# Optimization experiments

Hardware: AMD Instinct MI355X
Metric: run time of the kernel (lower is better)

Reference implementation:

```python
import jax, jax.numpy as jnp
import numpy as np

VOCAB = 21128; EMBED = 768; D_MODEL = 256; H = 100; NTAGS = 21; B = 32; T = 256


def setup_inputs() -> dict:
    key = jax.random.key(0)
    ks = jax.random.split(key, 18)
    n = lambda k, s, sc=0.05: jax.random.normal(k, s, dtype=jnp.float32) * sc
    return {
        "words": jax.random.randint(ks[0], (B, T), 0, VOCAB),
        "target": jax.random.randint(ks[1], (B, T), 0, NTAGS),
        "embed_table": n(ks[2], (VOCAB, EMBED), 1.0),
        "in_fc_w": n(ks[3], (D_MODEL, EMBED)),
        "in_fc_b": n(ks[4], (D_MODEL,)),
        "Wih0": n(ks[5], (2, 4 * H, D_MODEL)),
        "Whh0": n(ks[6], (2, 4 * H, H)),
        "bih0": n(ks[7], (2, 4 * H)),
        "bhh0": n(ks[8], (2, 4 * H)),
        "Wih1": n(ks[9], (2, 4 * H, 2 * H)),
        "Whh1": n(ks[10], (2, 4 * H, H)),
        "bih1": n(ks[11], (2, 4 * H)),
        "bhh1": n(ks[12], (2, 4 * H)),
        "out_w": n(ks[13], (NTAGS, 2 * H)),
        "out_b": n(ks[14], (NTAGS,)),
        "trans": n(ks[15], (NTAGS, NTAGS)),
        "start_s": n(ks[16], (NTAGS,)),
        "end_s": n(ks[17], (NTAGS,)),
    }


def _lstm_dir(x, Wih, Whh, bih, bhh, reverse):
    # x: (T, B, D); torch LSTM gate order i, f, g, o
    Bsz, Hd = x.shape[1], Whh.shape[1]
    pre = jnp.einsum('tbd,gd->tbg', x, Wih) + bih  # precompute input projection

    def step(carry, p):
        h, c = carry
        g = p + h @ Whh.T + bhh
        i, f, gg, o = jnp.split(g, 4, axis=-1)
        c = jax.nn.sigmoid(f) * c + jax.nn.sigmoid(i) * jnp.tanh(gg)
        h = jax.nn.sigmoid(o) * jnp.tanh(c)
        return (h, c), h

    init = (jnp.zeros((Bsz, Hd), x.dtype), jnp.zeros((Bsz, Hd), x.dtype))
    _, hs = jax.lax.scan(step, init, pre, reverse=reverse)
    return hs


def _bilstm(x, layers):
    h = x
    for (Wih, Whh, bih, bhh) in layers:  # fixed small loop over num_layers
        f = _lstm_dir(h, Wih[0], Whh[0], bih[0], bhh[0], False)
        b = _lstm_dir(h, Wih[1], Whh[1], bih[1], bhh[1], True)
        h = jnp.concatenate([f, b], axis=-1)
    return h


def _crf_loss(logits, tags, mask, trans, start_s, end_s):
    # fastNLP ConditionalRandomField loss: normalizer - gold_score, per batch elem
    lt = jnp.swapaxes(logits, 0, 1)          # (T, B, N)
    tt = tags.T                               # (T, B)
    mt = mask.T.astype(logits.dtype)          # (T, B)
    alpha0 = lt[0] + start_s

    def step(alpha, inp):
        emit, m = inp
        tmp = alpha[:, :, None] + trans[None] + emit[:, None, :]  # (B, N, N)
        new = jax.nn.logsumexp(tmp, axis=1)
        return jnp.where(m[:, None] > 0, new, alpha), None

    alpha, _ = jax.lax.scan(step, alpha0, (lt[1:], mt[1:]))
    normalizer = jax.nn.logsumexp(alpha + end_s, axis=1)  # (B,)

    emit_sc = jnp.take_along_axis(lt, tt[..., None], axis=2)[..., 0] * mt
    trans_sc = trans[tt[:-1], tt[1:]] * mt[1:]
    seq_lens = mask.sum(axis=1)
    last_idx = jnp.maximum(seq_lens - 1, 0)
    last_tags = tags[jnp.arange(tags.shape[0]), last_idx]
    gold = emit_sc.sum(0) + trans_sc.sum(0) + start_s[tt[0]] + end_s[last_tags]
    return normalizer - gold


def reference(words, target, embed_table, in_fc_w, in_fc_b, Wih0, Whh0, bih0, bhh0,
              Wih1, Whh1, bih1, bhh1, out_w, out_b, trans, start_s, end_s):
    mask = words != 0
    x = embed_table[words]                       # (B, T, E)
    x = x @ in_fc_w.T + in_fc_b                  # (B, T, D)
    x = jnp.swapaxes(x, 0, 1)                    # (T, B, D)
    h = _bilstm(x, [(Wih0, Whh0, bih0, bhh0), (Wih1, Whh1, bih1, bhh1)])
    h = jnp.swapaxes(h, 0, 1)                    # (B, T, 2H); dropout is identity at eval
    logits = jax.nn.log_softmax(h @ out_w.T + out_b, axis=-1)
    return _crf_loss(logits, target, mask, trans, start_s, end_s)  # (B,)
```

## Files before the change

kernel.cpp:

```cpp
#include <hip/hip_runtime.h>
#include <hip/hip_bf16.h>

#define VOCAB 21128
#define EMBED 768
#define DMODEL 256
#define HID 100
#define NTAGS 21
#define BB 32
#define TT 256
#define NTOK (BB*TT)

typedef float f32x4 __attribute__((ext_vector_type(4)));
typedef unsigned int u32x4 __attribute__((ext_vector_type(4)));
typedef short s16x8 __attribute__((ext_vector_type(8)));

__device__ __forceinline__ float sigm(float x) { return 1.0f / (1.0f + __expf(-x)); }
__device__ __forceinline__ float tanh_(float x) { return 2.0f / (1.0f + __expf(-2.0f * x)) - 1.0f; }

__device__ __forceinline__ unsigned int bfr(float x) {
    unsigned int u = __float_as_uint(x);
    return (u + 0x7fffu + ((u >> 16) & 1u)) >> 16;
}
__device__ __forceinline__ unsigned int bfpack(float lo, float hi) {
    return (bfr(hi) << 16) | bfr(lo);
}
__device__ __forceinline__ s16x8 asfrag(u32x4 v) {
    union { u32x4 u; s16x8 s; } x; x.u = v; return x.s;
}

#define BARV(SB) do { \
    asm volatile("s_waitcnt lgkmcnt(0)" ::: "memory"); \
    __builtin_amdgcn_s_barrier(); \
    if (SB) __builtin_amdgcn_sched_barrier(0); \
} while (0)
#define BAR() BARV(1)

__global__ __launch_bounds__(256) void gemm_mfma(
    const float* __restrict__ A, int lda,
    const float* __restrict__ B, int ldb,
    const float* __restrict__ bias1, const float* __restrict__ bias2,
    float* __restrict__ C, int ldc,
    int N, int K,
    const int* __restrict__ gatherWords, int permGates)
{
    __shared__ unsigned int As_[2][4096];
    __shared__ unsigned int Bs_[2][2048];

    const int tid = threadIdx.x;
    const int row0 = blockIdx.x * 128;
    const int col0 = blockIdx.y * 64;
    const int lane = tid & 63;
    const int wave = tid >> 6;
    const int wr = wave >> 1, wc = wave & 1;
    const int nsteps = (K + 63) >> 6;

    const float* arow[8]; int aoff[8]; int kqA[8];
    #pragma unroll
    for (int j = 0; j < 8; ++j) {
        int v = tid + 256 * j;
        int row = v >> 4, kq = v & 15;
        int grow = row0 + row;
        const float* ap;
        if (gatherWords) {
            int widx = gatherWords[(grow & 31) * TT + (grow >> 5)];
            ap = A + (size_t)widx * lda;
        } else {
            ap = A + (size_t)grow * lda;
        }
        arow[j] = ap + 4 * kq;
        aoff[j] = (row >> 4) * 512 + (kq >> 3) * 256 + ((kq >> 1) & 3) * 64
                + (row & 15) * 4 + (kq & 1) * 2;
        kqA[j] = kq;
    }
    const float* brow[4]; int boff[4]; int bok[4]; int kqB[4];
    #pragma unroll
    for (int j = 0; j < 4; ++j) {
        int v = tid + 256 * j;
        int r = v >> 4, kq = v & 15;
        int gcol = col0 + r;
        bok[j] = (gcol < N);
        int src = bok[j] ? gcol : 0;
        if (permGates && bok[j]) {
            int d2 = (gcol >= 400) ? 1 : 0;
            int rr = gcol - d2 * 400;
            src = d2 * 400 + (rr & 3) * 100 + (rr >> 2);
        }
        brow[j] = B + (size_t)src * ldb + 4 * kq;
        boff[j] = (r >> 4) * 512 + (kq >> 3) * 256 + ((kq >> 1) & 3) * 64
                + (r & 15) * 4 + (kq & 1) * 2;
        kqB[j] = kq;
    }

    {
        #pragma unroll
        for (int j = 0; j < 8; ++j) {
            f32x4 v = {0.f,0.f,0.f,0.f};
            if (4 * kqA[j] < K) v = *(const f32x4*)(arow[j]);
            As_[0][aoff[j]]     = bfpack(v.x, v.y);
            As_[0][aoff[j] + 1] = bfpack(v.z, v.w);
        }
        #pragma unroll
        for (int j = 0; j < 4; ++j) {
            f32x4 v = {0.f,0.f,0.f,0.f};
            if (bok[j] && 4 * kqB[j] < K) v = *(const f32x4*)(brow[j]);
            Bs_[0][boff[j]]     = bfpack(v.x, v.y);
            Bs_[0][boff[j] + 1] = bfpack(v.z, v.w);
        }
    }
    BAR();

    f32x4 acc[4][2] = {};

    for (int s = 0; s < nsteps; ++s) {
        const int cur = s & 1, nxt = cur ^ 1;

        f32x4 la[8], lb[4];
        if (s + 1 < nsteps) {
            const int kb = (s + 1) * 64;
            #pragma unroll
            for (int j = 0; j < 8; ++j) {
                la[j] = (f32x4){0.f,0.f,0.f,0.f};
                if (kb + 4 * kqA[j] < K) la[j] = *(const f32x4*)(arow[j] + kb);
            }
            #pragma unroll
            for (int j = 0; j < 4; ++j) {
                lb[j] = (f32x4){0.f,0.f,0.f,0.f};
                if (bok[j] && kb + 4 * kqB[j] < K) lb[j] = *(const f32x4*)(brow[j] + kb);
            }
        }

        u32x4 af[2][4], bf2[2][2];
        #pragma unroll
        for (int f = 0; f < 2; ++f) {
            #pragma unroll
            for (int mt = 0; mt < 4; ++mt)
                af[f][mt] = *(const u32x4*)&As_[cur][(4 * wr + mt) * 512 + f * 256 + lane * 4];
            #pragma unroll
            for (int nt = 0; nt < 2; ++nt)
                bf2[f][nt] = *(const u32x4*)&Bs_[cur][(2 * wc + nt) * 512 + f * 256 + lane * 4];
        }
        #pragma unroll
        for (int f = 0; f < 2; ++f)
            #pragma unroll
            for (int mt = 0; mt < 4; ++mt)
                #pragma unroll
                for (int nt = 0; nt < 2; ++nt)
                    acc[mt][nt] = __builtin_amdgcn_mfma_f32_16x16x32_bf16(
                        asfrag(af[f][mt]), asfrag(bf2[f][nt]), acc[mt][nt], 0, 0, 0);

        if (s + 1 < nsteps) {
            #pragma unroll
            for (int j = 0; j < 8; ++j) {
                As_[nxt][aoff[j]]     = bfpack(la[j].x, la[j].y);
                As_[nxt][aoff[j] + 1] = bfpack(la[j].z, la[j].w);
            }
            #pragma unroll
            for (int j = 0; j < 4; ++j) {
                Bs_[nxt][boff[j]]     = bfpack(lb[j].x, lb[j].y);
                Bs_[nxt][boff[j] + 1] = bfpack(lb[j].z, lb[j].w);
            }
        }
        BAR();
    }

    const int r4 = (lane >> 4) * 4;
    const int cl = lane & 15;
    #pragma unroll
    for (int nt = 0; nt < 2; ++nt) {
        int gcol = col0 + (2 * wc + nt) * 16 + cl;
        if (gcol < N) {
            int src = gcol;
            if (permGates) {
                int d2 = (gcol >= 400) ? 1 : 0;
                int rr = gcol - d2 * 400;
                src = d2 * 400 + (rr & 3) * 100 + (rr >> 2);
            }
            float bv = bias1[src];
            if (bias2) bv += bias2[src];
            #pragma unroll
            for (int mt = 0; mt < 4; ++mt) {
                int grow = row0 + (4 * wr + mt) * 16 + r4;
                #pragma unroll
                for (int r = 0; r < 4; ++r)
                    C[(size_t)(grow + r) * ldc + gcol] = acc[mt][nt][r] + bv;
            }
        }
    }
}

#define STASH_FRAG(DD, F, A0,A1,A2,A3) { \
    int tile = 4*wave + DD; if (tile > 24) tile = 24; \
    int row16 = 16*tile + m16; \
    const float* srcp = Whh + (size_t)(dir*400 + (row16 & 3)*100 + (row16 >> 2)) * HID; \
    const int k0 = 32*F + 8*g4; \
    f32x4 fa = {0.f,0.f,0.f,0.f}, fb = {0.f,0.f,0.f,0.f}; \
    if (k0 < HID) fa = *(const f32x4*)(srcp + k0); \
    if (k0 + 4 < HID) fb = *(const f32x4*)(srcp + k0 + 4); \
    unsigned p0 = bfpack(fa.x, fa.y), p1 = bfpack(fa.z, fa.w); \
    unsigned p2 = bfpack(fb.x, fb.y), p3 = bfpack(fb.z, fb.w); \
    asm volatile("v_accvgpr_write_b32 a" #A0 ", %0\n\t" \
                 "v_accvgpr_write_b32 a" #A1 ", %1\n\t" \
                 "v_accvgpr_write_b32 a" #A2 ", %2\n\t" \
                 "v_accvgpr_write_b32 a" #A3 ", %3" \
                 :: "v"(p0), "v"(p1), "v"(p2), "v"(p3) \
                 : "a" #A0, "a" #A1, "a" #A2, "a" #A3); }

#define MF(ACC, BF, A0, A3) \
    asm volatile("v_mfma_f32_16x16x32_bf16 %0, a[" #A0 ":" #A3 "], %1, %0" \
                 : "+v"(ACC) : "v"(BF));

#define LOADCHUNK(K2) { \
    const int s0_ = 16 * (K2); \
    _Pragma("unroll") \
    for (int j = 0; j < 4; ++j) { \
        if (okj[j]) { \
            int tg = dir ? (TT - 1 - (s0_ + sicj[j])) : (s0_ + sicj[j]); \
            rr[j] = *(const f32x4*)(pre + (size_t)(tg * BB + b) * 800 + dir * 400 + 4 * gqj[j]); \
        } \
    } }

#define WRITECHUNK(BUF) { \
    _Pragma("unroll") \
    for (int j = 0; j < 4; ++j) { \
        if (okj[j]) *(f32x4*)&preS[(BUF) * 6400 + sicj[j] * 400 + 4 * gqj[j]] = rr[j]; \
    } }

#define LSTM_STEP(SIC) { \
    const int t_ = dir ? (TT - 1 - (s0 + (SIC))) : (s0 + (SIC)); \
    const int i_ = t_ * BB + b; \
    const u32x4* hb_ = (const u32x4*)&h16[(SIC) & 1][0]; \
    u32x4 bf0 = hb_[g4], bf1 = hb_[4+g4], bf2 = hb_[8+g4], bf3 = hb_[12+g4]; \
    f32x4 p4 = *(const f32x4*)&preS[curbase + (SIC) * 400 + my_po]; \
    f32x4 acc0 = {0.f,0.f,0.f,0.f}, acc1 = {0.f,0.f,0.f,0.f}; \
    f32x4 acc2 = {0.f,0.f,0.f,0.f}, acc3 = {0.f,0.f,0.f,0.f}; \
    asm volatile("s_nop 1"); \
    MF(acc0, bf0, 0, 3)   MF(acc1, bf0, 16, 19) MF(acc2, bf0, 32, 35) MF(acc3, bf0, 48, 51) \
    MF(acc0, bf1, 4, 7)   MF(acc1, bf1, 20, 23) MF(acc2, bf1, 36, 39) MF(acc3, bf1, 52, 55) \
    MF(acc0, bf2, 8, 11)  MF(acc1, bf2, 24, 27) MF(acc2, bf2, 40, 43) MF(acc3, bf2, 56, 59) \
    MF(acc0, bf3, 12, 15) MF(acc1, bf3, 28, 31) MF(acc2, bf3, 44, 47) MF(acc3, bf3, 60, 63) \
    asm volatile("s_nop 7\n\ts_nop 7"); \
    f32x4 sel = (d == 0) ? acc0 : (d == 1) ? acc1 : (d == 2) ? acc2 : acc3; \
    float igt = sigm(sel.x + p4.x); \
    float fgt = sigm(sel.y + p4.y); \
    float ggt = tanh_(sel.z + p4.z); \
    float ogt = sigm(sel.w + p4.w); \
    c = fgt * c + igt * ggt; \
    float h = ogt * tanh_(c); \
    if (writer) { \
        h16[((SIC) + 1) & 1][my_u] = (unsigned short)bfr(h); \
        hout[(size_t)i_ * 200 + dir * HID + my_u] = h; \
    } \
    BARV(VAR == 0); }

template<int VAR>
__global__ __launch_bounds__(448, 1) void lstm_mfma(
    const float* __restrict__ pre,
    const float* __restrict__ Whh,
    float* __restrict__ hout)
{
    const int dir = blockIdx.x >> 5;
    const int b = blockIdx.x & 31;
    const int tid = threadIdx.x;
    const int wave = tid >> 6;
    const int lane = tid & 63;
    const int m16 = lane & 15;
    const int g4 = lane >> 4;
    const int d = lane & 3;

    __shared__ alignas(16) unsigned short h16[2][128];
    __shared__ alignas(16) float preS[2 * 6400];

    STASH_FRAG(0,0, 0,1,2,3)    STASH_FRAG(0,1, 4,5,6,7)
    STASH_FRAG(0,2, 8,9,10,11)  STASH_FRAG(0,3, 12,13,14,15)
    STASH_FRAG(1,0, 16,17,18,19) STASH_FRAG(1,1, 20,21,22,23)
    STASH_FRAG(1,2, 24,25,26,27) STASH_FRAG(1,3, 28,29,30,31)
    STASH_FRAG(2,0, 32,33,34,35) STASH_FRAG(2,1, 36,37,38,39)
    STASH_FRAG(2,2, 40,41,42,43) STASH_FRAG(2,3, 44,45,46,47)
    STASH_FRAG(3,0, 48,49,50,51) STASH_FRAG(3,1, 52,53,54,55)
    STASH_FRAG(3,2, 56,57,58,59) STASH_FRAG(3,3, 60,61,62,63)

    if (tid < 128) { h16[0][tid] = 0; h16[1][tid] = 0; }

    int my_tile = 4 * wave + d; if (my_tile > 24) my_tile = 24;
    const int my_u = my_tile * 4 + g4;
    const int my_po = 16 * my_tile + 4 * g4;
    const bool writer = ((lane & 12) == 0) && (wave < 6 || d == 0);

    int sicj[4], gqj[4]; bool okj[4];
    #pragma unroll
    for (int j = 0; j < 4; ++j) {
        int idx = tid + 448 * j;
        okj[j] = (idx < 1600);
        int ic = okj[j] ? idx : 0;
        sicj[j] = ic / 100;
        gqj[j] = ic - 100 * sicj[j];
    }

    float c = 0.f;
    f32x4 rr[4];

    LOADCHUNK(0)
    WRITECHUNK(0)
    LOADCHUNK(1)
    BAR();

    for (int k = 0; k < 16; ++k) {
        const int s0 = 16 * k;
        const int curbase = (k & 1) * 6400;
        LSTM_STEP(0)  LSTM_STEP(1)  LSTM_STEP(2)  LSTM_STEP(3)
        LSTM_STEP(4)  LSTM_STEP(5)  LSTM_STEP(6)  LSTM_STEP(7)
        LSTM_STEP(8)  LSTM_STEP(9)  LSTM_STEP(10) LSTM_STEP(11)
        LSTM_STEP(12) LSTM_STEP(13) LSTM_STEP(14) LSTM_STEP(15)
        if (k < 15) { WRITECHUNK((k & 1) ^ 1) }
        if (k < 14) { LOADCHUNK(k + 2) }
        BAR();
    }
}

__global__ __launch_bounds__(256) void logits_lsm(
    const float* __restrict__ h1,
    const float* __restrict__ out_w,
    const float* __restrict__ out_b,
    float* __restrict__ logits)
{
    const int lane = threadIdx.x & 63;
    const int wid = (blockIdx.x * 256 + threadIdx.x) >> 6;
    const int half = lane >> 5;
    const int n = lane & 31;
    const int i = wid * 2 + half;
    if (i >= NTOK) return;

    float acc = -1e30f;
    if (n < NTAGS) {
        acc = out_b[n];
        const float4* hr = (const float4*)(h1 + (size_t)i * 200);
        const float4* wr = (const float4*)(out_w + (size_t)n * 200);
        #pragma unroll
        for (int e = 0; e < 50; ++e) {
            float4 h4 = hr[e], w4 = wr[e];
            acc += h4.x * w4.x + h4.y * w4.y + h4.z * w4.z + h4.w * w4.w;
        }
    }
    float m = acc;
    for (int off = 16; off > 0; off >>= 1) m = fmaxf(m, __shfl_xor(m, off, 32));
    float ex = (n < NTAGS) ? __expf(acc - m) : 0.f;
    float s = ex;
    for (int off = 16; off > 0; off >>= 1) s += __shfl_xor(s, off, 32);
    if (n < NTAGS) logits[(size_t)i * NTAGS + n] = acc - m - __logf(s);
}

__global__ __launch_bounds__(64) void crf_kernel(
    const float* __restrict__ logits,
    const int* __restrict__ words,
    const int* __restrict__ target,
    const float* __restrict__ trans,
    const float* __restrict__ start_s,
    const float* __restrict__ end_s,
    float* __restrict__ out)
{
    const int b = blockIdx.x;
    const int j = threadIdx.x;
    const int j21 = (j < NTAGS) ? j : (NTAGS - 1);

    float tcol[NTAGS];
    #pragma unroll
    for (int i = 0; i < NTAGS; ++i) tcol[i] = (j < NTAGS) ? trans[i * NTAGS + j] : 0.f;

    const int w0 = words[b * TT +   0 + j];
    const int w1 = words[b * TT +  64 + j];
    const int w2 = words[b * TT + 128 + j];
    const int w3 = words[b * TT + 192 + j];

    float alpha = (j < NTAGS) ? (logits[(size_t)(0 * BB + b) * NTAGS + j] + start_s[j]) : -1e30f;
    float e_cur = logits[(size_t)(1 * BB + b) * NTAGS + j21];

#define CRF_CHUNK(WREG, T0) \
    for (int u = ((T0) == 0 ? 1 : 0); u < 64; ++u) { \
        const int t = (T0) + u; \
        float e_nxt = 0.f; \
        if (t + 1 < TT) e_nxt = logits[(size_t)((t + 1) * BB + b) * NTAGS + j21]; \
        if (__shfl(WREG, u, 64) != 0) { \
            float v[NTAGS]; \
            _Pragma("unroll") \
            for (int i2 = 0; i2 < NTAGS; ++i2) \
                v[i2] = __shfl(alpha, i2, 64) + tcol[i2]; \
            float m0[11]; \
            _Pragma("unroll") \
            for (int p = 0; p < 10; ++p) m0[p] = fmaxf(v[2*p], v[2*p+1]); \
            m0[10] = v[20]; \
            float m1[6]; \
            _Pragma("unroll") \
            for (int p = 0; p < 5; ++p) m1[p] = fmaxf(m0[2*p], m0[2*p+1]); \
            m1[5] = m0[10]; \
            float m2a = fmaxf(m1[0], m1[1]), m2b = fmaxf(m1[2], m1[3]), m2c = fmaxf(m1[4], m1[5]); \
            float mx = fmaxf(fmaxf(m2a, m2b), m2c); \
            float e[NTAGS]; \
            _Pragma("unroll") \
            for (int i2 = 0; i2 < NTAGS; ++i2) e[i2] = __expf(v[i2] - mx); \
            float s0[11]; \
            _Pragma("unroll") \
            for (int p = 0; p < 10; ++p) s0[p] = e[2*p] + e[2*p+1]; \
            s0[10] = e[20]; \
            float s1[6]; \
            _Pragma("unroll") \
            for (int p = 0; p < 5; ++p) s1[p] = s0[2*p] + s0[2*p+1]; \
            s1[5] = s0[10]; \
            float ss = ((s1[0] + s1[1]) + (s1[2] + s1[3])) + (s1[4] + s1[5]); \
            float na = mx + __logf(ss) + e_cur; \
            alpha = (j < NTAGS) ? na : -1e30f; \
        } \
        e_cur = e_nxt; \
    }

    CRF_CHUNK(w0, 0)
    CRF_CHUNK(w1, 64)
    CRF_CHUNK(w2, 128)
    CRF_CHUNK(w3, 192)
#undef CRF_CHUNK

    float val = (j < NTAGS) ? (alpha + end_s[j]) : -1e30f;
    float mx = val;
    for (int off = 32; off > 0; off >>= 1) mx = fmaxf(mx, __shfl_xor(mx, off, 64));
    float s = (j < NTAGS) ? __expf(val - mx) : 0.f;
    for (int off = 32; off > 0; off >>= 1) s += __shfl_xor(s, off, 64);
    float norm = mx + __logf(s);

    float gold = 0.f, slen = 0.f;
    for (int t = j; t < TT; t += 64) {
        int tg = target[b * TT + t];
        bool m = (words[b * TT + t] != 0);
        if (m) {
            gold += logits[(size_t)(t * BB + b) * NTAGS + tg];
            slen += 1.f;
            if (t >= 1) gold += trans[target[b * TT + t - 1] * NTAGS + tg];
        }
    }
    for (int off = 32; off > 0; off >>= 1) {
        gold += __shfl_xor(gold, off, 64);
        slen += __shfl_xor(slen, off, 64);
    }
    if (j == 0) {
        int len = (int)slen;
        int last = (len > 0) ? (len - 1) : 0;
        int last_tag = target[b * TT + last];
        gold += start_s[target[b * TT + 0]] + end_s[last_tag];
        out[b] = norm - gold;
    }
}

extern "C" void kernel_launch(void* const* d_in, const int* in_sizes, int n_in,
                              void* d_out, int out_size, void* d_ws, size_t ws_size,
                              hipStream_t stream) {
    const int*   words   = (const int*)  d_in[0];
    const int*   target  = (const int*)  d_in[1];
    const float* embed   = (const float*)d_in[2];
    const float* in_fc_w = (const float*)d_in[3];
    const float* in_fc_b = (const float*)d_in[4];
    const float* Wih0    = (const float*)d_in[5];
    const float* Whh0    = (const float*)d_in[6];
    const float* bih0    = (const float*)d_in[7];
    const float* bhh0    = (const float*)d_in[8];
    const float* Wih1    = (const float*)d_in[9];
    const float* Whh1    = (const float*)d_in[10];
    const float* bih1    = (const float*)d_in[11];
    const float* bhh1    = (const float*)d_in[12];
    const float* out_w   = (const float*)d_in[13];
    const float* out_b   = (const float*)d_in[14];
    const float* trans   = (const float*)d_in[15];
    const float* start_s = (const float*)d_in[16];
    const float* end_s   = (const float*)d_in[17];
    float* out = (float*)d_out;

    float* ws = (float*)d_ws;
    float* x      = ws;
    float* pre    = ws + 2097152;
    float* h0     = ws + 8650752;
    float* h1     = ws;
    float* logits = ws + 1638400;

    gemm_mfma<<<dim3(64, 4), 256, 0, stream>>>(
        embed, EMBED, in_fc_w, EMBED, in_fc_b, nullptr,
        x, DMODEL, DMODEL, EMBED, words, 0);

    gemm_mfma<<<dim3(64, 13), 256, 0, stream>>>(
        x, DMODEL, Wih0, DMODEL, bih0, bhh0,
        pre, 800, 800, DMODEL, nullptr, 1);

    lstm_mfma<0><<<64, 448, 0, stream>>>(pre, Whh0, h0);

    gemm_mfma<<<dim3(64, 13), 256, 0, stream>>>(
        h0, 200, Wih1, 200, bih1, bhh1,
        pre, 800, 800, 200, nullptr, 1);

    lstm_mfma<1><<<64, 448, 0, stream>>>(pre, Whh1, h1);

    logits_lsm<<<NTOK / 8, 256, 0, stream>>>(h1, out_w, out_b, logits);

    crf_kernel<<<BB, 64, 0, stream>>>(logits, words, target, trans, start_s, end_s, out);
}
```

Before: 582.6 us.

## Shrink LSTM recurrence block to 4 waves with 7 MFMA tiles per wave

The recurrent LSTM kernel moves from 7 waves (448 threads, 4 gate tiles each) to 4 waves (256 threads) that each own 6–7 of the 25 16-row Whh tiles, kept in AGPRs. Fewer waves makes the per-timestep block barrier cheaper, at the cost of a longer serial MFMA chain per wave (28 instead of 16) and more AGPR and register pressure. The preactivation chunk loader now does 7 loads per thread instead of 4, and the template variant that disabled the sched barrier is removed.

```diff
diff --git a/kernel.cpp b/kernel.cpp
--- a/kernel.cpp
+++ b/kernel.cpp
@@ -28,12 +28,11 @@
     union { u32x4 u; s16x8 s; } x; x.u = v; return x.s;
 }
 
-#define BARV(SB) do { \
+#define BAR() do { \
     asm volatile("s_waitcnt lgkmcnt(0)" ::: "memory"); \
     __builtin_amdgcn_s_barrier(); \
-    if (SB) __builtin_amdgcn_sched_barrier(0); \
+    __builtin_amdgcn_sched_barrier(0); \
 } while (0)
-#define BAR() BARV(1)
 
 __global__ __launch_bounds__(256) void gemm_mfma(
     const float* __restrict__ A, int lda,
@@ -188,11 +187,11 @@
     }
 }
 
-#define STASH_FRAG(DD, F, A0,A1,A2,A3) { \
-    int tile = 4*wave + DD; if (tile > 24) tile = 24; \
+#define STASH_FRAG(SS, F, A0,A1,A2,A3) { \
+    int tile = base + (SS); if (tile > 24) tile = 24; \
     int row16 = 16*tile + m16; \
     const float* srcp = Whh + (size_t)(dir*400 + (row16 & 3)*100 + (row16 >> 2)) * HID; \
-    const int k0 = 32*F + 8*g4; \
+    const int k0 = 32*(F) + 8*g4; \
     f32x4 fa = {0.f,0.f,0.f,0.f}, fb = {0.f,0.f,0.f,0.f}; \
     if (k0 < HID) fa = *(const f32x4*)(srcp + k0); \
     if (k0 + 4 < HID) fb = *(const f32x4*)(srcp + k0 + 4); \
@@ -212,7 +211,7 @@
 #define LOADCHUNK(K2) { \
     const int s0_ = 16 * (K2); \
     _Pragma("unroll") \
-    for (int j = 0; j < 4; ++j) { \
+    for (int j = 0; j < 7; ++j) { \
         if (okj[j]) { \
             int tg = dir ? (TT - 1 - (s0_ + sicj[j])) : (s0_ + sicj[j]); \
             rr[j] = *(const f32x4*)(pre + (size_t)(tg * BB + b) * 800 + dir * 400 + 4 * gqj[j]); \
@@ -221,7 +220,7 @@
 
 #define WRITECHUNK(BUF) { \
     _Pragma("unroll") \
-    for (int j = 0; j < 4; ++j) { \
+    for (int j = 0; j < 7; ++j) { \
         if (okj[j]) *(f32x4*)&preS[(BUF) * 6400 + sicj[j] * 400 + 4 * gqj[j]] = rr[j]; \
     } }
 
@@ -233,13 +232,28 @@
     f32x4 p4 = *(const f32x4*)&preS[curbase + (SIC) * 400 + my_po]; \
     f32x4 acc0 = {0.f,0.f,0.f,0.f}, acc1 = {0.f,0.f,0.f,0.f}; \
     f32x4 acc2 = {0.f,0.f,0.f,0.f}, acc3 = {0.f,0.f,0.f,0.f}; \
+    f32x4 acc4 = {0.f,0.f,0.f,0.f}, acc5 = {0.f,0.f,0.f,0.f}; \
+    f32x4 acc6 = {0.f,0.f,0.f,0.f}; \
     asm volatile("s_nop 1"); \
-    MF(acc0, bf0, 0, 3)   MF(acc1, bf0, 16, 19) MF(acc2, bf0, 32, 35) MF(acc3, bf0, 48, 51) \
-    MF(acc0, bf1, 4, 7)   MF(acc1, bf1, 20, 23) MF(acc2, bf1, 36, 39) MF(acc3, bf1, 52, 55) \
-    MF(acc0, bf2, 8, 11)  MF(acc1, bf2, 24, 27) MF(acc2, bf2, 40, 43) MF(acc3, bf2, 56, 59) \
-    MF(acc0, bf3, 12, 15) MF(acc1, bf3, 28, 31) MF(acc2, bf3, 44, 47) MF(acc3, bf3, 60, 63) \
+    MF(acc0, bf0, 0, 3)    MF(acc1, bf0, 16, 19)  MF(acc2, bf0, 32, 35) \
+    MF(acc3, bf0, 48, 51)  MF(acc4, bf0, 64, 67)  MF(acc5, bf0, 80, 83) \
+    MF(acc6, bf0, 96, 99) \
+    MF(acc0, bf1, 4, 7)    MF(acc1, bf1, 20, 23)  MF(acc2, bf1, 36, 39) \
+    MF(acc3, bf1, 52, 55)  MF(acc4, bf1, 68, 71)  MF(acc5, bf1, 84, 87) \
+    MF(acc6, bf1, 100, 103) \
+    MF(acc0, bf2, 8, 11)   MF(acc1, bf2, 24, 27)  MF(acc2, bf2, 40, 43) \
+    MF(acc3, bf2, 56, 59)  MF(acc4, bf2, 72, 75)  MF(acc5, bf2, 88, 91) \
+    MF(acc6, bf2, 104, 107) \
+    MF(acc0, bf3, 12, 15)  MF(acc1, bf3, 28, 31)  MF(acc2, bf3, 44, 47) \
+    MF(acc3, bf3, 60, 63)  MF(acc4, bf3, 76, 79)  MF(acc5, bf3, 92, 95) \
+    MF(acc6, bf3, 108, 111) \
     asm volatile("s_nop 7\n\ts_nop 7"); \
-    f32x4 sel = (d == 0) ? acc0 : (d == 1) ? acc1 : (d == 2) ? acc2 : acc3; \
+    f32x4 t01 = (slot_sel & 1) ? acc1 : acc0; \
+    f32x4 t23 = (slot_sel & 1) ? acc3 : acc2; \
+    f32x4 t45 = (slot_sel & 1) ? acc5 : acc4; \
+    f32x4 u0 = (slot_sel & 2) ? t23 : t01; \
+    f32x4 u1 = (slot_sel & 2) ? acc6 : t45; \
+    f32x4 sel = (slot_sel & 4) ? u1 : u0; \
     float igt = sigm(sel.x + p4.x); \
     float fgt = sigm(sel.y + p4.y); \
     float ggt = tanh_(sel.z + p4.z); \
@@ -250,10 +264,9 @@
         h16[((SIC) + 1) & 1][my_u] = (unsigned short)bfr(h); \
         hout[(size_t)i_ * 200 + dir * HID + my_u] = h; \
     } \
-    BARV(VAR == 0); }
-
-template<int VAR>
-__global__ __launch_bounds__(448, 1) void lstm_mfma(
+    BAR(); }
+
+__global__ __launch_bounds__(256, 1) void lstm_mfma(
     const float* __restrict__ pre,
     const float* __restrict__ Whh,
     float* __restrict__ hout)
@@ -265,31 +278,41 @@
     const int lane = tid & 63;
     const int m16 = lane & 15;
     const int g4 = lane >> 4;
-    const int d = lane & 3;
+    const int slot_sel = lane & 7;
+
+    const int base = (wave == 0) ? 0 : (wave == 1) ? 7 : (wave == 2) ? 13 : 19;
 
     __shared__ alignas(16) unsigned short h16[2][128];
     __shared__ alignas(16) float preS[2 * 6400];
 
-    STASH_FRAG(0,0, 0,1,2,3)    STASH_FRAG(0,1, 4,5,6,7)
-    STASH_FRAG(0,2, 8,9,10,11)  STASH_FRAG(0,3, 12,13,14,15)
-    STASH_FRAG(1,0, 16,17,18,19) STASH_FRAG(1,1, 20,21,22,23)
-    STASH_FRAG(1,2, 24,25,26,27) STASH_FRAG(1,3, 28,29,30,31)
-    STASH_FRAG(2,0, 32,33,34,35) STASH_FRAG(2,1, 36,37,38,39)
-    STASH_FRAG(2,2, 40,41,42,43) STASH_FRAG(2,3, 44,45,46,47)
-    STASH_FRAG(3,0, 48,49,50,51) STASH_FRAG(3,1, 52,53,54,55)
-    STASH_FRAG(3,2, 56,57,58,59) STASH_FRAG(3,3, 60,61,62,63)
+    STASH_FRAG(0,0, 0,1,2,3)      STASH_FRAG(0,1, 4,5,6,7)
+    STASH_FRAG(0,2, 8,9,10,11)    STASH_FRAG(0,3, 12,13,14,15)
+    STASH_FRAG(1,0, 16,17,18,19)  STASH_FRAG(1,1, 20,21,22,23)
+    STASH_FRAG(1,2, 24,25,26,27)  STASH_FRAG(1,3, 28,29,30,31)
+    STASH_FRAG(2,0, 32,33,34,35)  STASH_FRAG(2,1, 36,37,38,39)
+    STASH_FRAG(2,2, 40,41,42,43)  STASH_FRAG(2,3, 44,45,46,47)
+    STASH_FRAG(3,0, 48,49,50,51)  STASH_FRAG(3,1, 52,53,54,55)
+    STASH_FRAG(3,2, 56,57,58,59)  STASH_FRAG(3,3, 60,61,62,63)
+    STASH_FRAG(4,0, 64,65,66,67)  STASH_FRAG(4,1, 68,69,70,71)
+    STASH_FRAG(4,2, 72,73,74,75)  STASH_FRAG(4,3, 76,77,78,79)
+    STASH_FRAG(5,0, 80,81,82,83)  STASH_FRAG(5,1, 84,85,86,87)
+    STASH_FRAG(5,2, 88,89,90,91)  STASH_FRAG(5,3, 92,93,94,95)
+    STASH_FRAG(6,0, 96,97,98,99)  STASH_FRAG(6,1, 100,101,102,103)
+    STASH_FRAG(6,2, 104,105,106,107) STASH_FRAG(6,3, 108,109,110,111)
 
     if (tid < 128) { h16[0][tid] = 0; h16[1][tid] = 0; }
 
-    int my_tile = 4 * wave + d; if (my_tile > 24) my_tile = 24;
-    const int my_u = my_tile * 4 + g4;
+    int my_tile = base + ((slot_sel < 7) ? slot_sel : 6);
+    if (my_tile > 24) my_tile = 24;
+    const int my_u = 4 * my_tile + g4;
     const int my_po = 16 * my_tile + 4 * g4;
-    const bool writer = ((lane & 12) == 0) && (wave < 6 || d == 0);
-
-    int sicj[4], gqj[4]; bool okj[4];
+    const int ow_lim = (wave == 0) ? 7 : 6;
+    const bool writer = (slot_sel < ow_lim) && ((lane & 8) == 0);
+
+    int sicj[7], gqj[7]; bool okj[7];
     #pragma unroll
-    for (int j = 0; j < 4; ++j) {
-        int idx = tid + 448 * j;
+    for (int j = 0; j < 7; ++j) {
+        int idx = tid + 256 * j;
         okj[j] = (idx < 1600);
         int ic = okj[j] ? idx : 0;
         sicj[j] = ic / 100;
@@ -297,7 +320,7 @@
     }
 
     float c = 0.f;
-    f32x4 rr[4];
+    f32x4 rr[7];
 
     LOADCHUNK(0)
     WRITECHUNK(0)
@@ -486,13 +509,13 @@
         x, DMODEL, Wih0, DMODEL, bih0, bhh0,
         pre, 800, 800, DMODEL, nullptr, 1);
 
-    lstm_mfma<0><<<64, 448, 0, stream>>>(pre, Whh0, h0);
+    lstm_mfma<<<64, 256, 0, stream>>>(pre, Whh0, h0);
 
     gemm_mfma<<<dim3(64, 13), 256, 0, stream>>>(
         h0, 200, Wih1, 200, bih1, bhh1,
         pre, 800, 800, 200, nullptr, 1);
 
-    lstm_mfma<1><<<64, 448, 0, stream>>>(pre, Whh1, h1);
+    lstm_mfma<<<64, 256, 0, stream>>>(pre, Whh1, h1);
 
     logits_lsm<<<NTOK / 8, 256, 0, stream>>>(h1, out_w, out_b, logits);
 
```

New measurement: 559.9 us, median of 3. 1.04x faster.
